# Kernel tuning notes

Measured on AMD Instinct MI355X. Metric: run time of the kernel, lower is better.

## Reference

```python
import jax, jax.numpy as jnp
import numpy as np


def setup_inputs() -> dict:
    key = jax.random.key(0)
    k1, k2 = jax.random.split(key)
    mat_1 = jax.random.normal(k1, (100000, 64), dtype=jnp.float32)
    mat_2 = jax.random.normal(k2, (2048, 64), dtype=jnp.float32)
    return {"mat_1": mat_1, "mat_2": mat_2}


def reference(mat_1, mat_2):
    # Squared euclidean distance between every row of mat_1 and mat_2.
    # Same math as sum((a - b)**2) = ||a||^2 + ||b||^2 - 2 a.b,
    # expressed as a single GEMM plus broadcast adds.
    sq1 = jnp.sum(mat_1 * mat_1, axis=1, keepdims=True)        # (n_1, 1)
    sq2 = jnp.sum(mat_2 * mat_2, axis=1)                       # (n_2,)
    cross = jnp.einsum('nd,md->nm', mat_1, mat_2)              # (n_1, n_2)
    dist = sq1 + sq2[None, :] - 2.0 * cross
    return dist
```

## Files before the change

### kernel.cpp

```cpp
#include <hip/hip_runtime.h>
#include <cstdint>
#include <cstddef>


typedef __bf16 v8bf __attribute__((ext_vector_type(8)));
typedef float  v4f  __attribute__((ext_vector_type(4)));

__device__ inline unsigned short f32_to_bf16_rne(float f) {
    union { float f; uint32_t u; } c; c.f = f;
    uint32_t u = c.u;
    uint32_t r = (u + 0x7fffu + ((u >> 16) & 1u)) >> 16;
    return (unsigned short)r;
}

__global__ __launch_bounds__(256) void prep_kernel(const float* __restrict__ B,
                                                   unsigned short* __restrict__ Bbf,
                                                   float* __restrict__ sq2, int N) {
    int t = blockIdx.x * 256 + threadIdx.x;
    int row = t >> 2;
    if (row >= N) return;
    int q = (t & 3) * 16;
    const float* src = B + (size_t)row * 64 + q;
    unsigned short* dst = Bbf + (size_t)row * 64 + q;
    float s = 0.f;
#pragma unroll
    for (int i = 0; i < 4; ++i) {
        float4 v = *reinterpret_cast<const float4*>(src + 4 * i);
        s += v.x * v.x + v.y * v.y + v.z * v.z + v.w * v.w;
        uint2 p;
        p.x = (uint32_t)f32_to_bf16_rne(-2.f * v.x) | ((uint32_t)f32_to_bf16_rne(-2.f * v.y) << 16);
        p.y = (uint32_t)f32_to_bf16_rne(-2.f * v.z) | ((uint32_t)f32_to_bf16_rne(-2.f * v.w) << 16);
        *reinterpret_cast<uint2*>(dst + 4 * i) = p;
    }
    s += __shfl_xor(s, 1);
    s += __shfl_xor(s, 2);
    if ((t & 3) == 0) sq2[row] = s;
}

__global__ __launch_bounds__(512, 1) void dist_kernel(const float* __restrict__ A,
                                                      const unsigned short* __restrict__ Bbf,
                                                      const float* __restrict__ sq2,
                                                      float* __restrict__ out,
                                                      int M, int N, int NT) {
    __shared__ __align__(16) unsigned char b_lds[131072];
    __shared__ __align__(16) float stage_lds[8][512];

    const int t = threadIdx.x;
    const int h = blockIdx.x >> 8;
    const int s = blockIdx.x & 255;
    const int NH = N >> 1;

    {
        const unsigned short* src = Bbf + (size_t)h * NH * 64;
        const int nchunk = NH * 8;
        for (int idx = t; idx < nchunk; idx += 512) {
            int col = idx >> 3, q = idx & 7;
            uint4 v = *reinterpret_cast<const uint4*>(src + col * 64 + q * 8);
            int L = col * 128 + q * 16;
            *reinterpret_cast<uint4*>(b_lds + (L ^ ((col & 7) << 4))) = v;
        }
    }
    __syncthreads();

    const int lane = t & 63;
    const int w    = t >> 6;
    const int lg   = lane >> 4;
    const int li   = lane & 15;
    const int swz  = (li & 7) << 4;
    float* const stg = &stage_lds[w][0];

    v4f s2v[2][4];
#pragma unroll
    for (int cc = 0; cc < 2; ++cc)
#pragma unroll
        for (int ct = 0; ct < 4; ++ct)
            s2v[cc][ct] = *reinterpret_cast<const v4f*>(
                &sq2[h * NH + cc * 512 + w * 64 + 16 * ct + 4 * lg]);

    v8bf bf[2][4][2];
#pragma unroll
    for (int cc = 0; cc < 2; ++cc)
#pragma unroll
        for (int ct = 0; ct < 4; ++ct)
#pragma unroll
            for (int kb = 0; kb < 2; ++kb) {
                int col = cc * 512 + w * 64 + 16 * ct + li;
                int L = col * 128 + kb * 64 + lg * 16;
                bf[cc][ct][kb] = *reinterpret_cast<const v8bf*>(b_lds + (L ^ swz));
            }

    float4 raw[8];
    auto loadA = [&](int tt) {
        const int m0 = tt * 32;
#pragma unroll
        for (int rt = 0; rt < 2; ++rt) {
            int r = m0 + 16 * rt + li; if (r >= M) r = M - 1;
            const float* ar = A + (size_t)r * 64;
#pragma unroll
            for (int kb = 0; kb < 2; ++kb) {
                raw[rt * 4 + kb * 2]     = *reinterpret_cast<const float4*>(ar + kb * 32 + 8 * lg);
                raw[rt * 4 + kb * 2 + 1] = *reinterpret_cast<const float4*>(ar + kb * 32 + 8 * lg + 4);
            }
        }
    };

    loadA(s);

#pragma unroll 1
    for (int tt = s; tt < NT; tt += 256) {
        const int m0 = tt * 32;

        v8bf  af[2][2];
        float s1[2];
#pragma unroll
        for (int rt = 0; rt < 2; ++rt) {
            float ss = 0.f;
#pragma unroll
            for (int kb = 0; kb < 2; ++kb) {
                float4 x0 = raw[rt * 4 + kb * 2];
                float4 x1 = raw[rt * 4 + kb * 2 + 1];
                ss += x0.x * x0.x + x0.y * x0.y + x0.z * x0.z + x0.w * x0.w;
                ss += x1.x * x1.x + x1.y * x1.y + x1.z * x1.z + x1.w * x1.w;
                union { v8bf v; unsigned short u[8]; } pk;
                pk.u[0] = f32_to_bf16_rne(x0.x); pk.u[1] = f32_to_bf16_rne(x0.y);
                pk.u[2] = f32_to_bf16_rne(x0.z); pk.u[3] = f32_to_bf16_rne(x0.w);
                pk.u[4] = f32_to_bf16_rne(x1.x); pk.u[5] = f32_to_bf16_rne(x1.y);
                pk.u[6] = f32_to_bf16_rne(x1.z); pk.u[7] = f32_to_bf16_rne(x1.w);
                af[rt][kb] = pk.v;
            }
            ss += __shfl_xor(ss, 16);
            ss += __shfl_xor(ss, 32);
            s1[rt] = ss;
        }

        {
            int tn = tt + 256; if (tn >= NT) tn = tt;
            loadA(tn);
        }

#pragma unroll
        for (int cc = 0; cc < 2; ++cc) {
            v4f acc[2][4];
#pragma unroll
            for (int rt = 0; rt < 2; ++rt)
#pragma unroll
                for (int ct = 0; ct < 4; ++ct)
                    acc[rt][ct] = s2v[cc][ct] + s1[rt];

#pragma unroll
            for (int rt = 0; rt < 2; ++rt)
#pragma unroll
                for (int ct = 0; ct < 4; ++ct) {
                    acc[rt][ct] = __builtin_amdgcn_mfma_f32_16x16x32_bf16(bf[cc][ct][0], af[rt][0], acc[rt][ct], 0, 0, 0);
                    acc[rt][ct] = __builtin_amdgcn_mfma_f32_16x16x32_bf16(bf[cc][ct][1], af[rt][1], acc[rt][ct], 0, 0, 0);
                }

            const int cbase = h * NH + cc * 512 + w * 64;
#pragma unroll
            for (int rt = 0; rt < 2; ++rt) {
#pragma unroll
                for (int hf = 0; hf < 2; ++hf) {
#pragma unroll
                    for (int q = 0; q < 2; ++q) {
                        int c = 16 * q + 4 * lg;
                        *reinterpret_cast<v4f*>(&stg[li * 32 + (c ^ (4 * (li & 7)))]) =
                            acc[rt][2 * hf + q];
                    }
#pragma unroll
                    for (int g = 0; g < 2; ++g) {
                        int r2 = 8 * g + (lane >> 3);
                        int c2 = 4 * (lane & 7);
                        v4f v = *reinterpret_cast<const v4f*>(
                            &stg[r2 * 32 + (c2 ^ (4 * (r2 & 7)))]);
                        int grow = m0 + 16 * rt + r2;
                        if (grow < M)
                            __builtin_nontemporal_store(v,
                                reinterpret_cast<v4f*>(out + (size_t)grow * N + cbase + 32 * hf + c2));
                    }
                }
            }
        }
    }
}

extern "C" void kernel_launch(void* const* d_in, const int* in_sizes, int n_in,
                              void* d_out, int out_size, void* d_ws, size_t ws_size,
                              hipStream_t stream) {
    const float* A = (const float*)d_in[0];
    const float* B = (const float*)d_in[1];
    const int M = in_sizes[0] / 64;
    const int N = in_sizes[1] / 64;

    unsigned short* Bbf = (unsigned short*)d_ws;
    float* sq2 = (float*)((char*)d_ws + (size_t)N * 64 * sizeof(unsigned short));
    float* out = (float*)d_out;

    prep_kernel<<<(N * 4 + 255) / 256, 256, 0, stream>>>(B, Bbf, sq2, N);

    const int NT = (M + 31) / 32;
    dist_kernel<<<512, 512, 0, stream>>>(A, Bbf, sq2, out, M, N, NT);
}
```

Baseline: 164.6 us.

## Fuse B conversion and norm computation into distance kernel, drop prep launch

Result: no change. 164.5 us (-0.1%).

```diff
diff --git a/kernel.cpp b/kernel.cpp
--- a/kernel.cpp
+++ b/kernel.cpp
@@ -12,55 +12,22 @@
     uint32_t r = (u + 0x7fffu + ((u >> 16) & 1u)) >> 16;
     return (unsigned short)r;
 }
-
-__global__ __launch_bounds__(256) void prep_kernel(const float* __restrict__ B,
-                                                   unsigned short* __restrict__ Bbf,
-                                                   float* __restrict__ sq2, int N) {
-    int t = blockIdx.x * 256 + threadIdx.x;
-    int row = t >> 2;
-    if (row >= N) return;
-    int q = (t & 3) * 16;
-    const float* src = B + (size_t)row * 64 + q;
-    unsigned short* dst = Bbf + (size_t)row * 64 + q;
-    float s = 0.f;
-#pragma unroll
-    for (int i = 0; i < 4; ++i) {
-        float4 v = *reinterpret_cast<const float4*>(src + 4 * i);
-        s += v.x * v.x + v.y * v.y + v.z * v.z + v.w * v.w;
-        uint2 p;
-        p.x = (uint32_t)f32_to_bf16_rne(-2.f * v.x) | ((uint32_t)f32_to_bf16_rne(-2.f * v.y) << 16);
-        p.y = (uint32_t)f32_to_bf16_rne(-2.f * v.z) | ((uint32_t)f32_to_bf16_rne(-2.f * v.w) << 16);
-        *reinterpret_cast<uint2*>(dst + 4 * i) = p;
-    }
-    s += __shfl_xor(s, 1);
-    s += __shfl_xor(s, 2);
-    if ((t & 3) == 0) sq2[row] = s;
+__device__ inline uint32_t pack2_m2(float a, float b) {
+    return (uint32_t)f32_to_bf16_rne(-2.f * a) | ((uint32_t)f32_to_bf16_rne(-2.f * b) << 16);
 }
 
 __global__ __launch_bounds__(512, 1) void dist_kernel(const float* __restrict__ A,
-                                                      const unsigned short* __restrict__ Bbf,
-                                                      const float* __restrict__ sq2,
+                                                      const float* __restrict__ B,
                                                       float* __restrict__ out,
                                                       int M, int N, int NT) {
     __shared__ __align__(16) unsigned char b_lds[131072];
     __shared__ __align__(16) float stage_lds[8][512];
+    __shared__ float sq2_lds[1024];
 
     const int t = threadIdx.x;
     const int h = blockIdx.x >> 8;
     const int s = blockIdx.x & 255;
     const int NH = N >> 1;
-
-    {
-        const unsigned short* src = Bbf + (size_t)h * NH * 64;
-        const int nchunk = NH * 8;
-        for (int idx = t; idx < nchunk; idx += 512) {
-            int col = idx >> 3, q = idx & 7;
-            uint4 v = *reinterpret_cast<const uint4*>(src + col * 64 + q * 8);
-            int L = col * 128 + q * 16;
-            *reinterpret_cast<uint4*>(b_lds + (L ^ ((col & 7) << 4))) = v;
-        }
-    }
-    __syncthreads();
 
     const int lane = t & 63;
     const int w    = t >> 6;
@@ -69,13 +36,51 @@
     const int swz  = (li & 7) << 4;
     float* const stg = &stage_lds[w][0];
 
+    float4 raw[8];
+    auto loadA = [&](int tt) {
+        const int m0 = tt * 32;
+#pragma unroll
+        for (int rt = 0; rt < 2; ++rt) {
+            const float* ar = A + (size_t)(m0 + 16 * rt + li) * 64;
+#pragma unroll
+            for (int kb = 0; kb < 2; ++kb) {
+                raw[rt * 4 + kb * 2]     = *reinterpret_cast<const float4*>(ar + kb * 32 + 8 * lg);
+                raw[rt * 4 + kb * 2 + 1] = *reinterpret_cast<const float4*>(ar + kb * 32 + 8 * lg + 4);
+            }
+        }
+    };
+    loadA(s);
+
+    {
+        const float* src = B + (size_t)h * NH * 64;
+        const int nchunk = NH * 8;
+#pragma unroll 1
+        for (int idx = t; idx < nchunk; idx += 512) {
+            int col = idx >> 3, q = idx & 7;
+            float4 x0 = *reinterpret_cast<const float4*>(src + col * 64 + q * 8);
+            float4 x1 = *reinterpret_cast<const float4*>(src + col * 64 + q * 8 + 4);
+            float ss = x0.x * x0.x + x0.y * x0.y + x0.z * x0.z + x0.w * x0.w
+                     + x1.x * x1.x + x1.y * x1.y + x1.z * x1.z + x1.w * x1.w;
+            uint4 v;
+            v.x = pack2_m2(x0.x, x0.y); v.y = pack2_m2(x0.z, x0.w);
+            v.z = pack2_m2(x1.x, x1.y); v.w = pack2_m2(x1.z, x1.w);
+            int L = col * 128 + q * 16;
+            *reinterpret_cast<uint4*>(b_lds + (L ^ ((col & 7) << 4))) = v;
+            ss += __shfl_xor(ss, 1);
+            ss += __shfl_xor(ss, 2);
+            ss += __shfl_xor(ss, 4);
+            if ((t & 7) == 0) sq2_lds[col] = ss;
+        }
+    }
+    __syncthreads();
+
     v4f s2v[2][4];
 #pragma unroll
     for (int cc = 0; cc < 2; ++cc)
 #pragma unroll
         for (int ct = 0; ct < 4; ++ct)
             s2v[cc][ct] = *reinterpret_cast<const v4f*>(
-                &sq2[h * NH + cc * 512 + w * 64 + 16 * ct + 4 * lg]);
+                &sq2_lds[cc * 512 + w * 64 + 16 * ct + 4 * lg]);
 
     v8bf bf[2][4][2];
 #pragma unroll
@@ -88,23 +93,6 @@
                 int L = col * 128 + kb * 64 + lg * 16;
                 bf[cc][ct][kb] = *reinterpret_cast<const v8bf*>(b_lds + (L ^ swz));
             }
-
-    float4 raw[8];
-    auto loadA = [&](int tt) {
-        const int m0 = tt * 32;
-#pragma unroll
-        for (int rt = 0; rt < 2; ++rt) {
-            int r = m0 + 16 * rt + li; if (r >= M) r = M - 1;
-            const float* ar = A + (size_t)r * 64;
-#pragma unroll
-            for (int kb = 0; kb < 2; ++kb) {
-                raw[rt * 4 + kb * 2]     = *reinterpret_cast<const float4*>(ar + kb * 32 + 8 * lg);
-                raw[rt * 4 + kb * 2 + 1] = *reinterpret_cast<const float4*>(ar + kb * 32 + 8 * lg + 4);
-            }
-        }
-    };
-
-    loadA(s);
 
 #pragma unroll 1
     for (int tt = s; tt < NT; tt += 256) {
@@ -172,10 +160,9 @@
                         int c2 = 4 * (lane & 7);
                         v4f v = *reinterpret_cast<const v4f*>(
                             &stg[r2 * 32 + (c2 ^ (4 * (r2 & 7)))]);
-                        int grow = m0 + 16 * rt + r2;
-                        if (grow < M)
-                            __builtin_nontemporal_store(v,
-                                reinterpret_cast<v4f*>(out + (size_t)grow * N + cbase + 32 * hf + c2));
+                        __builtin_nontemporal_store(v,
+                            reinterpret_cast<v4f*>(out + (size_t)(m0 + 16 * rt + r2) * N
+                                                   + cbase + 32 * hf + c2));
                     }
                 }
             }
@@ -190,13 +177,8 @@
     const float* B = (const float*)d_in[1];
     const int M = in_sizes[0] / 64;
     const int N = in_sizes[1] / 64;
-
-    unsigned short* Bbf = (unsigned short*)d_ws;
-    float* sq2 = (float*)((char*)d_ws + (size_t)N * 64 * sizeof(unsigned short));
     float* out = (float*)d_out;
 
-    prep_kernel<<<(N * 4 + 255) / 256, 256, 0, stream>>>(B, Bbf, sq2, N);
-
     const int NT = (M + 31) / 32;
-    dist_kernel<<<512, 512, 0, stream>>>(A, Bbf, sq2, out, M, N, NT);
+    dist_kernel<<<512, 512, 0, stream>>>(A, B, out, M, N, NT);
 }
```
